# Kernel tuning notes

Measured on AMD Instinct MI355X. Metric: run time of the kernel, lower is better.

## Reference

```python
import jax, jax.numpy as jnp
import numpy as np

D_MODEL = 1024
NUM_HEADS = 16
D_HEAD = D_MODEL // NUM_HEADS


def rotate_half(x):
    half = x.shape[-1] // 2
    x1, x2 = x[..., :half], x[..., half:]
    return jnp.concatenate((-x2, x1), axis=-1)


def rope_cos_sin(seq_len, d_head, dtype):
    # inv_freq over even dims of d_head
    inv_freq = 1.0 / (10000.0 ** (jnp.arange(0, d_head, 2, dtype=jnp.float32) / d_head))
    t = jnp.arange(seq_len, dtype=jnp.float32)
    freqs = jnp.einsum('i,j->ij', t, inv_freq)        # [L, d_head/2]
    emb = jnp.concatenate((freqs, freqs), axis=-1)    # [L, d_head]
    return jnp.cos(emb).astype(dtype), jnp.sin(emb).astype(dtype)


def setup_inputs() -> dict:
    key = jax.random.key(0)
    ks = jax.random.split(key, 9)
    B, L = 2, 2048
    s = 1.0 / np.sqrt(D_MODEL)
    return {
        'x': jax.random.normal(ks[0], (B, L, D_MODEL), dtype=jnp.float32),
        'Wq': jax.random.normal(ks[1], (D_MODEL, D_MODEL), dtype=jnp.float32) * s,
        'bq': jax.random.normal(ks[2], (D_MODEL,), dtype=jnp.float32) * 0.02,
        'Wk': jax.random.normal(ks[3], (D_MODEL, D_MODEL), dtype=jnp.float32) * s,
        'bk': jax.random.normal(ks[4], (D_MODEL,), dtype=jnp.float32) * 0.02,
        'Wv': jax.random.normal(ks[5], (D_MODEL, D_MODEL), dtype=jnp.float32) * s,
        'bv': jax.random.normal(ks[6], (D_MODEL,), dtype=jnp.float32) * 0.02,
        'Wo': jax.random.normal(ks[7], (D_MODEL, D_MODEL), dtype=jnp.float32) * s,
        'bo': jax.random.normal(ks[8], (D_MODEL,), dtype=jnp.float32) * 0.02,
    }


def reference(x, Wq, bq, Wk, bk, Wv, bv, Wo, bo):
    B, L, D = x.shape
    H, Dh = NUM_HEADS, D_HEAD
    scale = Dh ** -0.5

    # projections: torch Linear is x @ W.T + b; here W stored as [in, out]-like
    # square matrices, so treat Wq etc. directly as x @ Wq + bq.
    q = (x @ Wq + bq).reshape(B, L, H, Dh).transpose(0, 2, 1, 3)  # [B,H,L,Dh]
    k = (x @ Wk + bk).reshape(B, L, H, Dh).transpose(0, 2, 1, 3)
    v = (x @ Wv + bv).reshape(B, L, H, Dh).transpose(0, 2, 1, 3)

    cos, sin = rope_cos_sin(L, Dh, x.dtype)  # [L, Dh]
    cos = cos[None, None]  # [1,1,L,Dh]
    sin = sin[None, None]
    q = q * cos + rotate_half(q) * sin
    k = k * cos + rotate_half(k) * sin

    attn = jnp.einsum('bhqd,bhkd->bhqk', q, k) * scale  # [B,H,L,L]
    attn = jax.nn.softmax(attn, axis=-1)
    out = jnp.einsum('bhqk,bhkd->bhqd', attn, v)        # [B,H,L,Dh]
    out = out.transpose(0, 2, 1, 3).reshape(B, L, D)
    return out @ Wo + bo
```

## Files before the change

kernel.cpp:

```cpp
#include <hip/hip_runtime.h>
#include <cmath>

#define D_MODEL  1024
#define NHEADS   16
#define DHEAD    64
#define BATCH    2
#define SEQ      2048
#define MROWS    (BATCH * SEQ)
#define HALF_DH  32
#define BHTOT    (BATCH * NHEADS)
#define QROWS    (BHTOT * SEQ)

typedef __attribute__((ext_vector_type(8))) short short8;
typedef __attribute__((ext_vector_type(4))) float f32x4;
typedef __attribute__((ext_vector_type(16))) float f32x16;

#define MFMA16(A,B,C) __builtin_amdgcn_mfma_f32_16x16x32_bf16(A,B,C,0,0,0)
#define MFMA32(A,B,C) __builtin_amdgcn_mfma_f32_32x32x16_bf16(A,B,C,0,0,0)

__device__ __forceinline__ unsigned short f2bf(float f) {
    unsigned int u = __float_as_uint(f);
    u += 0x7fffu + ((u >> 16) & 1u);
    return (unsigned short)(u >> 16);
}

__device__ __forceinline__ void gload_lds16(const void* g, void* l) {
    __builtin_amdgcn_global_load_lds(
        (const __attribute__((address_space(1))) unsigned int*)g,
        (__attribute__((address_space(3))) unsigned int*)l,
        16, 0, 0);
}

__global__ __launch_bounds__(256)
void prep_kernel(const float* __restrict__ x,
                 const float* __restrict__ Wq, const float* __restrict__ Wk,
                 const float* __restrict__ Wv, const float* __restrict__ Wo,
                 unsigned short* __restrict__ xb,
                 unsigned short* __restrict__ wqT, unsigned short* __restrict__ wkT,
                 unsigned short* __restrict__ wvT, unsigned short* __restrict__ woT,
                 float* __restrict__ cosT, float* __restrict__ sinT)
{
    __shared__ unsigned short T[64][68];
    const int bid = blockIdx.x;
    const int tid = threadIdx.x;

    if (bid < 4096) {
        int i = bid * 256 + tid;
        float4 v = ((const float4*)x)[i];
        ushort4 o;
        o.x = f2bf(v.x); o.y = f2bf(v.y); o.z = f2bf(v.z); o.w = f2bf(v.w);
        ((ushort4*)xb)[i] = o;
    } else if (bid < 5120) {
        int b2 = bid - 4096;
        int z  = b2 >> 8;
        int bx = (b2 & 255) >> 4;
        int by = b2 & 15;
        const float* W; unsigned short* Wt;
        switch (z) {
            case 0:  W = Wq; Wt = wqT; break;
            case 1:  W = Wk; Wt = wkT; break;
            case 2:  W = Wv; Wt = wvT; break;
            default: W = Wo; Wt = woT; break;
        }
        const int k0 = bx * 64, n0 = by * 64;
        const int r = tid >> 4, cq = tid & 15;
        #pragma unroll
        for (int p = 0; p < 4; ++p) {
            int kk = r + 16 * p;
            float4 vv = *(const float4*)&W[(size_t)(k0 + kk) * D_MODEL + n0 + cq * 4];
            T[cq * 4 + 0][kk] = f2bf(vv.x);
            T[cq * 4 + 1][kk] = f2bf(vv.y);
            T[cq * 4 + 2][kk] = f2bf(vv.z);
            T[cq * 4 + 3][kk] = f2bf(vv.w);
        }
        __syncthreads();
        #pragma unroll
        for (int p = 0; p < 4; ++p) {
            int n = r + 16 * p;
            ushort4 ov;
            ov.x = T[n][cq * 4 + 0]; ov.y = T[n][cq * 4 + 1];
            ov.z = T[n][cq * 4 + 2]; ov.w = T[n][cq * 4 + 3];
            *(ushort4*)&Wt[(size_t)(n0 + n) * D_MODEL + k0 + cq * 4] = ov;
        }
    } else {
        int idx = (bid - 5120) * 256 + tid;
        int l = idx >> 5;
        int j = idx & 31;
        float inv = powf(10000.0f, -(float)(2 * j) / (float)DHEAD);
        float ang = (float)l * inv;
        cosT[idx] = cosf(ang);
        sinT[idx] = sinf(ang);
    }
}

__global__ __launch_bounds__(256)
void qkv_proj_kernel(const unsigned short* __restrict__ A,
                     const unsigned short* __restrict__ wqT, const unsigned short* __restrict__ wkT,
                     const unsigned short* __restrict__ wvT,
                     const float* __restrict__ bq, const float* __restrict__ bk,
                     const float* __restrict__ bv,
                     const float* __restrict__ cosT, const float* __restrict__ sinT,
                     unsigned short* __restrict__ qb, unsigned short* __restrict__ kb,
                     unsigned short* __restrict__ vtb)
{
    __shared__ unsigned short SMEM[128 * 64 + 64 * 64];
    unsigned short* As = SMEM;
    unsigned short* Bs = SMEM + 128 * 64;

    const int z = blockIdx.z;
    const unsigned short* Bt = (z == 0) ? wqT : (z == 1) ? wkT : wvT;
    const float* bias = (z == 0) ? bq : (z == 1) ? bk : bv;

    const int tid = threadIdx.x;
    const int w = tid >> 6, ln = tid & 63;
    const int c = ln & 15, g = ln >> 4;
    const int bm = blockIdx.x * 128, bn = blockIdx.y * 64;
    const int srow = ln >> 3, sblk = ln & 7;

    f32x4 acc[2][4];
    #pragma unroll
    for (int mi = 0; mi < 2; ++mi)
        #pragma unroll
        for (int ni = 0; ni < 4; ++ni) acc[mi][ni] = (f32x4){0.f, 0.f, 0.f, 0.f};

    for (int k0 = 0; k0 < D_MODEL; k0 += 64) {
        __syncthreads();
        #pragma unroll
        for (int i = 0; i < 4; ++i) {
            int chunk = w * 4 + i;
            int row = chunk * 8 + srow;
            int gcol = (sblk ^ (row & 7)) * 8;
            gload_lds16(&A[(size_t)(bm + row) * D_MODEL + k0 + gcol], &As[chunk * 512]);
        }
        #pragma unroll
        for (int i = 0; i < 2; ++i) {
            int chunk = w * 2 + i;
            int row = chunk * 8 + srow;
            int gcol = (sblk ^ (row & 7)) * 8;
            gload_lds16(&Bt[(size_t)(bn + row) * D_MODEL + k0 + gcol], &Bs[chunk * 512]);
        }
        __syncthreads();

        #pragma unroll
        for (int ks = 0; ks < 2; ++ks) {
            const int koff = (ks * 32 + g * 8) ^ ((c & 7) * 8);
            short8 af[2];
            #pragma unroll
            for (int mi = 0; mi < 2; ++mi)
                af[mi] = *(const short8*)&As[(w * 32 + mi * 16 + c) * 64 + koff];
            #pragma unroll
            for (int ni = 0; ni < 4; ++ni) {
                short8 bfr = *(const short8*)&Bs[(ni * 16 + c) * 64 + koff];
                #pragma unroll
                for (int mi = 0; mi < 2; ++mi)
                    acc[mi][ni] = MFMA16(af[mi], bfr, acc[mi][ni]);
            }
        }
    }

    float bv4[4];
    #pragma unroll
    for (int ni = 0; ni < 4; ++ni) bv4[ni] = bias[bn + ni * 16 + c];

    if (z < 2) {
        unsigned short* op = z ? kb : qb;
        const int hy = blockIdx.y;
        #pragma unroll
        for (int mi = 0; mi < 2; ++mi) {
            #pragma unroll
            for (int r = 0; r < 4; ++r) {
                const int m = bm + w * 32 + mi * 16 + g * 4 + r;
                const int b = m >> 11, ll = m & (SEQ - 1);
                float v[4];
                #pragma unroll
                for (int ni = 0; ni < 4; ++ni) v[ni] = acc[mi][ni][r] + bv4[ni];
                #pragma unroll
                for (int ni = 0; ni < 2; ++ni) {
                    int d = ni * 16 + c;
                    float co = cosT[ll * HALF_DH + d];
                    float si = sinT[ll * HALF_DH + d];
                    float lo = v[ni], hi = v[ni + 2];
                    v[ni]     = lo * co - hi * si;
                    v[ni + 2] = hi * co + lo * si;
                }
                unsigned short* dst = op + ((size_t)(b * NHEADS + hy) * SEQ + ll) * DHEAD;
                #pragma unroll
                for (int ni = 0; ni < 4; ++ni) dst[ni * 16 + c] = f2bf(v[ni]);
            }
        }
    } else {
        unsigned short (*T)[136] = (unsigned short(*)[136])SMEM;
        __syncthreads();
        #pragma unroll
        for (int mi = 0; mi < 2; ++mi)
            #pragma unroll
            for (int r = 0; r < 4; ++r)
                #pragma unroll
                for (int ni = 0; ni < 4; ++ni)
                    T[ni * 16 + c][w * 32 + mi * 16 + g * 4 + r] = f2bf(acc[mi][ni][r] + bv4[ni]);
        __syncthreads();
        const int b  = bm >> 11;
        const int l0 = bm & (SEQ - 1);
        const int bh = b * NHEADS + blockIdx.y;
        unsigned short* Vo = vtb + (size_t)bh * DHEAD * SEQ;
        #pragma unroll
        for (int it = 0; it < 4; ++it) {
            int row  = (tid >> 4) + it * 16;
            int col8 = tid & 15;
            uint4 val = *(const uint4*)&T[row][col8 * 8];
            *(uint4*)&Vo[(size_t)row * SEQ + l0 + col8 * 8] = val;
        }
    }
}

__global__ __launch_bounds__(256)
void outproj_kernel(const unsigned short* __restrict__ A, const unsigned short* __restrict__ Bt,
                    const float* __restrict__ bias, float* __restrict__ out)
{
    __shared__ unsigned short As[128 * 64];
    __shared__ unsigned short Bs[64 * 64];
    const int tid = threadIdx.x;
    const int w = tid >> 6, ln = tid & 63;
    const int c = ln & 15, g = ln >> 4;
    const int bm = blockIdx.x * 128, bn = blockIdx.y * 64;
    const int srow = ln >> 3, sblk = ln & 7;

    f32x4 acc[2][4];
    #pragma unroll
    for (int mi = 0; mi < 2; ++mi)
        #pragma unroll
        for (int ni = 0; ni < 4; ++ni) acc[mi][ni] = (f32x4){0.f, 0.f, 0.f, 0.f};

    for (int k0 = 0; k0 < D_MODEL; k0 += 64) {
        __syncthreads();
        #pragma unroll
        for (int i = 0; i < 4; ++i) {
            int chunk = w * 4 + i;
            int row = chunk * 8 + srow;
            int gcol = (sblk ^ (row & 7)) * 8;
            gload_lds16(&A[(size_t)(bm + row) * D_MODEL + k0 + gcol], &As[chunk * 512]);
        }
        #pragma unroll
        for (int i = 0; i < 2; ++i) {
            int chunk = w * 2 + i;
            int row = chunk * 8 + srow;
            int gcol = (sblk ^ (row & 7)) * 8;
            gload_lds16(&Bt[(size_t)(bn + row) * D_MODEL + k0 + gcol], &Bs[chunk * 512]);
        }
        __syncthreads();

        #pragma unroll
        for (int ks = 0; ks < 2; ++ks) {
            const int koff = (ks * 32 + g * 8) ^ ((c & 7) * 8);
            short8 af[2];
            #pragma unroll
            for (int mi = 0; mi < 2; ++mi)
                af[mi] = *(const short8*)&As[(w * 32 + mi * 16 + c) * 64 + koff];
            #pragma unroll
            for (int ni = 0; ni < 4; ++ni) {
                short8 bfr = *(const short8*)&Bs[(ni * 16 + c) * 64 + koff];
                #pragma unroll
                for (int mi = 0; mi < 2; ++mi)
                    acc[mi][ni] = MFMA16(af[mi], bfr, acc[mi][ni]);
            }
        }
    }

    float bv4[4];
    #pragma unroll
    for (int ni = 0; ni < 4; ++ni) bv4[ni] = bias[bn + ni * 16 + c];
    #pragma unroll
    for (int mi = 0; mi < 2; ++mi)
        #pragma unroll
        for (int r = 0; r < 4; ++r) {
            const int m = bm + w * 32 + mi * 16 + g * 4 + r;
            #pragma unroll
            for (int ni = 0; ni < 4; ++ni)
                out[(size_t)m * D_MODEL + bn + ni * 16 + c] = acc[mi][ni][r] + bv4[ni];
        }
}

__global__ __launch_bounds__(256, 4)
void attn_mfma32_kernel(const unsigned short* __restrict__ Q, const unsigned short* __restrict__ K,
                        const unsigned short* __restrict__ Vt, unsigned short* __restrict__ O,
                        float* __restrict__ accP, float* __restrict__ ml, int nsplit)
{
    __shared__ unsigned short Ks[2][64 * 64];
    __shared__ unsigned short Vs[2][64 * 64];
    const int tid = threadIdx.x;
    const int w = tid >> 6, ln = tid & 63;
    const int ql = ln & 31;
    const int h  = ln >> 5;
    const int bh = blockIdx.y;
    const int q  = blockIdx.x * 128 + w * 32 + ql;
    const int split = blockIdx.z;
    const int ntile = SEQ / (64 * nsplit);
    const int kt0 = split * (SEQ / nsplit);
    const float SC = 0.125f * 1.44269504088896340736f;
    const int srow = ln >> 3, sblk = ln & 7;

    const unsigned short* Qb = Q  + (size_t)bh * SEQ * DHEAD;
    const unsigned short* Kb = K  + (size_t)bh * SEQ * DHEAD;
    const unsigned short* Vb = Vt + (size_t)bh * DHEAD * SEQ;

    short8 qf[4];
    #pragma unroll
    for (int dk = 0; dk < 4; ++dk)
        qf[dk] = *(const short8*)&Qb[(size_t)q * DHEAD + dk * 16 + h * 8];

    short8 onesF;
    #pragma unroll
    for (int i = 0; i < 8; ++i) onesF[i] = (short)0x3F80;

    int offk[4];
    #pragma unroll
    for (int t = 0; t < 4; ++t) offk[t] = ((2 * t + h) ^ (ql & 7)) * 8;
    const int rA = ql * 64, rB = (32 + ql) * 64;

    f32x16 accO0, accO1, accS;
    #pragma unroll
    for (int r = 0; r < 16; ++r) { accO0[r] = 0.f; accO1[r] = 0.f; accS[r] = 0.f; }
    float mst = -1e30f;

    #pragma unroll
    for (int i = 0; i < 2; ++i) {
        int chunk = w * 2 + i;
        int row = chunk * 8 + srow;
        int gcol = (sblk ^ (row & 7)) * 8;
        gload_lds16(&Kb[(size_t)(kt0 + row) * DHEAD + gcol], &Ks[0][chunk * 512]);
        gload_lds16(&Vb[(size_t)row * SEQ + kt0 + gcol],     &Vs[0][chunk * 512]);
    }
    __syncthreads();

    int cur = 0;
    for (int it = 0; it < ntile; ++it) {
        const int kt = kt0 + it * 64;
        if (it + 1 < ntile) {
            #pragma unroll
            for (int i = 0; i < 2; ++i) {
                int chunk = w * 2 + i;
                int row = chunk * 8 + srow;
                int gcol = (sblk ^ (row & 7)) * 8;
                gload_lds16(&Kb[(size_t)(kt + 64 + row) * DHEAD + gcol], &Ks[cur ^ 1][chunk * 512]);
                gload_lds16(&Vb[(size_t)row * SEQ + kt + 64 + gcol],     &Vs[cur ^ 1][chunk * 512]);
            }
        }

        f32x16 s0, s1;
        #pragma unroll
        for (int r = 0; r < 16; ++r) { s0[r] = 0.f; s1[r] = 0.f; }
        #pragma unroll
        for (int dk = 0; dk < 4; ++dk) {
            short8 kf0 = *(const short8*)&Ks[cur][rA + offk[dk]];
            short8 kf1 = *(const short8*)&Ks[cur][rB + offk[dk]];
            s0 = MFMA32(kf0, qf[dk], s0);
            s1 = MFMA32(kf1, qf[dk], s1);
        }

        float a0 = fmaxf(fmaxf(s0[0], s0[1]), s0[2]);
        float a1 = fmaxf(fmaxf(s0[3], s0[4]), s0[5]);
        float a2 = fmaxf(fmaxf(s0[6], s0[7]), s0[8]);
        float a3 = fmaxf(fmaxf(s0[9], s0[10]), s0[11]);
        float a4 = fmaxf(fmaxf(s0[12], s0[13]), s0[14]);
        float a5 = fmaxf(fmaxf(s0[15], s1[0]), s1[1]);
        float a6 = fmaxf(fmaxf(s1[2], s1[3]), s1[4]);
        float a7 = fmaxf(fmaxf(s1[5], s1[6]), s1[7]);
        float a8 = fmaxf(fmaxf(s1[8], s1[9]), s1[10]);
        float a9 = fmaxf(fmaxf(s1[11], s1[12]), s1[13]);
        float aA = fmaxf(s1[14], s1[15]);
        float b0 = fmaxf(fmaxf(a0, a1), a2);
        float b1 = fmaxf(fmaxf(a3, a4), a5);
        float b2 = fmaxf(fmaxf(a6, a7), a8);
        float b3 = fmaxf(a9, aA);
        float mx = fmaxf(fmaxf(fmaxf(b0, b1), b2), b3);
        mx = fmaxf(mx, __shfl_xor(mx, 32));

        const float mn = fmaxf(mst, mx);
        const float rsc = exp2f((mst - mn) * SC);
        #pragma unroll
        for (int r = 0; r < 16; ++r) { accO0[r] *= rsc; accO1[r] *= rsc; }
        accS[0] *= rsc;
        mst = mn;

        #pragma unroll
        for (int r = 0; r < 16; ++r) {
            s0[r] = exp2f((s0[r] - mst) * SC);
            s1[r] = exp2f((s1[r] - mst) * SC);
        }

        short8 pf[4];
        #define REPACK_T(T, SV)                                                          \
        {                                                                                \
            unsigned int wA0, wA1, wB0, wB1;                                             \
            asm("v_cvt_pk_bf16_f32 %0, %1, %2" : "=v"(wA0)                               \
                : "v"((SV)[8 * ((T) & 1) + 0]), "v"((SV)[8 * ((T) & 1) + 1]));           \
            asm("v_cvt_pk_bf16_f32 %0, %1, %2" : "=v"(wA1)                               \
                : "v"((SV)[8 * ((T) & 1) + 2]), "v"((SV)[8 * ((T) & 1) + 3]));           \
            asm("v_cvt_pk_bf16_f32 %0, %1, %2" : "=v"(wB0)                               \
                : "v"((SV)[8 * ((T) & 1) + 4]), "v"((SV)[8 * ((T) & 1) + 5]));           \
            asm("v_cvt_pk_bf16_f32 %0, %1, %2" : "=v"(wB1)                               \
                : "v"((SV)[8 * ((T) & 1) + 6]), "v"((SV)[8 * ((T) & 1) + 7]));           \
            asm("v_permlane32_swap_b32 %0, %1" : "+v"(wA0), "+v"(wB0));                  \
            asm("v_permlane32_swap_b32 %0, %1" : "+v"(wA1), "+v"(wB1));                  \
            union { short8 v; unsigned int u[4]; } tmp;                                  \
            tmp.u[0] = wA0; tmp.u[1] = wA1; tmp.u[2] = wB0; tmp.u[3] = wB1;              \
            pf[T] = tmp.v;                                                               \
        }
        REPACK_T(0, s0) REPACK_T(1, s0) REPACK_T(2, s1) REPACK_T(3, s1)
        #undef REPACK_T

        #pragma unroll
        for (int t = 0; t < 4; ++t) {
            short8 vf0 = *(const short8*)&Vs[cur][rA + offk[t]];
            short8 vf1 = *(const short8*)&Vs[cur][rB + offk[t]];
            accS  = MFMA32(onesF, pf[t], accS);
            accO0 = MFMA32(vf0, pf[t], accO0);
            accO1 = MFMA32(vf1, pf[t], accO1);
        }

        __syncthreads();
        cur ^= 1;
    }

    const float accL = accS[0];
    if (nsplit == 1) {
        const int b = bh >> 4, hh = bh & 15;
        const float inv = 1.0f / accL;
        unsigned short* dst = O + ((size_t)(b * SEQ + q)) * D_MODEL + hh * DHEAD;
        #define EPI(ACC, DC)                                                             \
        {                                                                                \
            _Pragma("unroll")                                                            \
            for (int rq = 0; rq < 4; ++rq) {                                             \
                float a0 = (ACC)[4 * rq + 0] * inv, a1 = (ACC)[4 * rq + 1] * inv;        \
                float a2 = (ACC)[4 * rq + 2] * inv, a3 = (ACC)[4 * rq + 3] * inv;        \
                unsigned int p0, p1;                                                     \
                asm("v_cvt_pk_bf16_f32 %0, %1, %2" : "=v"(p0) : "v"(a0), "v"(a1));       \
                asm("v_cvt_pk_bf16_f32 %0, %1, %2" : "=v"(p1) : "v"(a2), "v"(a3));       \
                uint2 pk; pk.x = p0; pk.y = p1;                                          \
                *(uint2*)(dst + 32 * (DC) + 8 * rq + 4 * h) = pk;                        \
            }                                                                            \
        }
        EPI(accO0, 0) EPI(accO1, 1)
        #undef EPI
    } else {
        float* base = accP + ((size_t)(split * BHTOT + bh) * SEQ + q) * 64;
        #pragma unroll
        for (int rq = 0; rq < 4; ++rq) {
            float4 v0, v1;
            v0.x = accO0[4 * rq + 0]; v0.y = accO0[4 * rq + 1];
            v0.z = accO0[4 * rq + 2]; v0.w = accO0[4 * rq + 3];
            v1.x = accO1[4 * rq + 0]; v1.y = accO1[4 * rq + 1];
            v1.z = accO1[4 * rq + 2]; v1.w = accO1[4 * rq + 3];
            *(float4*)&base[8 * rq + 4 * h]      = v0;
            *(float4*)&base[32 + 8 * rq + 4 * h] = v1;
        }
        if (h == 0) {
            float2 v; v.x = mst; v.y = accL;
            ((float2*)ml)[(size_t)(split * BHTOT + bh) * SEQ + q] = v;
        }
    }
}

__global__ __launch_bounds__(256)
void combine2_kernel(const float* __restrict__ accP, const float* __restrict__ ml,
                     unsigned short* __restrict__ ob)
{
    const float SC = 0.125f * 1.44269504088896340736f;
    int t = blockIdx.x * 256 + threadIdx.x;
    int d4  = (t & 15) * 4;
    int bhq = t >> 4;
    const float2* ML = (const float2*)ml;
    float2 m0 = ML[bhq];
    float2 m1 = ML[(size_t)QROWS + bhq];
    float M  = fmaxf(m0.x, m1.x);
    float w0 = exp2f((m0.x - M) * SC);
    float w1 = exp2f((m1.x - M) * SC);
    float inv = 1.0f / (w0 * m0.y + w1 * m1.y);
    float4 a0 = *(const float4*)&accP[(size_t)bhq * 64 + d4];
    float4 a1 = *(const float4*)&accP[(size_t)QROWS * 64 + (size_t)bhq * 64 + d4];
    float o0 = (a0.x * w0 + a1.x * w1) * inv;
    float o1 = (a0.y * w0 + a1.y * w1) * inv;
    float o2 = (a0.z * w0 + a1.z * w1) * inv;
    float o3 = (a0.w * w0 + a1.w * w1) * inv;
    int bh = bhq >> 11, q = bhq & (SEQ - 1);
    int b = bh >> 4, hh = bh & 15;
    ushort4 ov;
    ov.x = f2bf(o0); ov.y = f2bf(o1); ov.z = f2bf(o2); ov.w = f2bf(o3);
    *(ushort4*)&ob[((size_t)(b * SEQ + q)) * D_MODEL + hh * DHEAD + d4] = ov;
}

extern "C" void kernel_launch(void* const* d_in, const int* in_sizes, int n_in,
                              void* d_out, int out_size, void* d_ws, size_t ws_size,
                              hipStream_t stream)
{
    const float* x  = (const float*)d_in[0];
    const float* Wq = (const float*)d_in[1];
    const float* bq = (const float*)d_in[2];
    const float* Wk = (const float*)d_in[3];
    const float* bk = (const float*)d_in[4];
    const float* Wv = (const float*)d_in[5];
    const float* bv = (const float*)d_in[6];
    const float* Wo = (const float*)d_in[7];
    const float* bo = (const float*)d_in[8];

    char* p = (char*)d_ws;
    float* cosT = (float*)p;            p += (size_t)SEQ * HALF_DH * 4;
    float* sinT = (float*)p;            p += (size_t)SEQ * HALF_DH * 4;
    unsigned short* xb  = (unsigned short*)p; p += (size_t)MROWS * D_MODEL * 2;
    unsigned short* wqT = (unsigned short*)p; p += (size_t)D_MODEL * D_MODEL * 2;
    unsigned short* wkT = (unsigned short*)p; p += (size_t)D_MODEL * D_MODEL * 2;
    unsigned short* wvT = (unsigned short*)p; p += (size_t)D_MODEL * D_MODEL * 2;
    unsigned short* woT = (unsigned short*)p; p += (size_t)D_MODEL * D_MODEL * 2;
    unsigned short* qb  = (unsigned short*)p; p += (size_t)MROWS * D_MODEL * 2;
    unsigned short* kb  = (unsigned short*)p; p += (size_t)MROWS * D_MODEL * 2;
    unsigned short* vtb = (unsigned short*)p; p += (size_t)MROWS * D_MODEL * 2;
    unsigned short* ob  = (unsigned short*)p; p += (size_t)MROWS * D_MODEL * 2;
    float* accP = (float*)p;            p += (size_t)2 * QROWS * 64 * 4;
    float* ml   = (float*)p;            p += (size_t)2 * QROWS * 2 * 4;
    size_t need2 = (size_t)(p - (char*)d_ws);
    const int nsplit = (ws_size >= need2) ? 2 : 1;

    prep_kernel<<<5376, 256, 0, stream>>>(x, Wq, Wk, Wv, Wo,
                                          xb, wqT, wkT, wvT, woT, cosT, sinT);

    qkv_proj_kernel<<<dim3(MROWS / 128, D_MODEL / 64, 3), 256, 0, stream>>>(
        xb, wqT, wkT, wvT, bq, bk, bv, cosT, sinT, qb, kb, vtb);

    attn_mfma32_kernel<<<dim3(SEQ / 128, BHTOT, nsplit), 256, 0, stream>>>(
        qb, kb, vtb, ob, accP, ml, nsplit);

    if (nsplit == 2)
        combine2_kernel<<<(QROWS * 16) / 256, 256, 0, stream>>>(accP, ml, ob);

    outproj_kernel<<<dim3(MROWS / 128, D_MODEL / 64), 256, 0, stream>>>(ob, woT, bo, (float*)d_out);
}
```

Measured before the change: 151.9 us.

## Widen projection GEMM tiles to 128 columns and skip rescale when max grows little

The QKV and output projection kernels now compute 128x128 tiles instead of 128x64, doubling accumulators per wave and halving the grid, so each A tile loaded into LDS feeds twice as much MFMA work. The epilogues are restructured to handle two heads per block, including the V transpose via shared memory done per head. Separately, the attention kernel now skips the online-softmax rescale unless some lane's max grows by more than a threshold, which avoids many multiplies but lets exponent arguments exceed zero by up to that bound. The larger tile raises register and LDS use and halves the block count, which can reduce occupancy.

```diff
diff --git a/kernel.cpp b/kernel.cpp
--- a/kernel.cpp
+++ b/kernel.cpp
@@ -103,7 +103,7 @@
                      unsigned short* __restrict__ qb, unsigned short* __restrict__ kb,
                      unsigned short* __restrict__ vtb)
 {
-    __shared__ unsigned short SMEM[128 * 64 + 64 * 64];
+    __shared__ unsigned short SMEM[128 * 64 + 128 * 64];
     unsigned short* As = SMEM;
     unsigned short* Bs = SMEM + 128 * 64;
 
@@ -114,14 +114,14 @@
     const int tid = threadIdx.x;
     const int w = tid >> 6, ln = tid & 63;
     const int c = ln & 15, g = ln >> 4;
-    const int bm = blockIdx.x * 128, bn = blockIdx.y * 64;
+    const int bm = blockIdx.x * 128, bn = blockIdx.y * 128;
     const int srow = ln >> 3, sblk = ln & 7;
 
-    f32x4 acc[2][4];
+    f32x4 acc[2][8];
     #pragma unroll
     for (int mi = 0; mi < 2; ++mi)
         #pragma unroll
-        for (int ni = 0; ni < 4; ++ni) acc[mi][ni] = (f32x4){0.f, 0.f, 0.f, 0.f};
+        for (int ni = 0; ni < 8; ++ni) acc[mi][ni] = (f32x4){0.f, 0.f, 0.f, 0.f};
 
     for (int k0 = 0; k0 < D_MODEL; k0 += 64) {
         __syncthreads();
@@ -133,8 +133,8 @@
             gload_lds16(&A[(size_t)(bm + row) * D_MODEL + k0 + gcol], &As[chunk * 512]);
         }
         #pragma unroll
-        for (int i = 0; i < 2; ++i) {
-            int chunk = w * 2 + i;
+        for (int i = 0; i < 4; ++i) {
+            int chunk = w * 4 + i;
             int row = chunk * 8 + srow;
             int gcol = (sblk ^ (row & 7)) * 8;
             gload_lds16(&Bt[(size_t)(bn + row) * D_MODEL + k0 + gcol], &Bs[chunk * 512]);
@@ -149,7 +149,7 @@
             for (int mi = 0; mi < 2; ++mi)
                 af[mi] = *(const short8*)&As[(w * 32 + mi * 16 + c) * 64 + koff];
             #pragma unroll
-            for (int ni = 0; ni < 4; ++ni) {
+            for (int ni = 0; ni < 8; ++ni) {
                 short8 bfr = *(const short8*)&Bs[(ni * 16 + c) * 64 + koff];
                 #pragma unroll
                 for (int mi = 0; mi < 2; ++mi)
@@ -158,57 +158,69 @@
         }
     }
 
-    float bv4[4];
-    #pragma unroll
-    for (int ni = 0; ni < 4; ++ni) bv4[ni] = bias[bn + ni * 16 + c];
+    float bv8[8];
+    #pragma unroll
+    for (int ni = 0; ni < 8; ++ni) bv8[ni] = bias[bn + ni * 16 + c];
 
     if (z < 2) {
         unsigned short* op = z ? kb : qb;
-        const int hy = blockIdx.y;
+        const int h0 = bn >> 6;
         #pragma unroll
         for (int mi = 0; mi < 2; ++mi) {
             #pragma unroll
             for (int r = 0; r < 4; ++r) {
                 const int m = bm + w * 32 + mi * 16 + g * 4 + r;
                 const int b = m >> 11, ll = m & (SEQ - 1);
-                float v[4];
+                float v[8];
                 #pragma unroll
-                for (int ni = 0; ni < 4; ++ni) v[ni] = acc[mi][ni][r] + bv4[ni];
+                for (int ni = 0; ni < 8; ++ni) v[ni] = acc[mi][ni][r] + bv8[ni];
                 #pragma unroll
-                for (int ni = 0; ni < 2; ++ni) {
-                    int d = ni * 16 + c;
-                    float co = cosT[ll * HALF_DH + d];
-                    float si = sinT[ll * HALF_DH + d];
-                    float lo = v[ni], hi = v[ni + 2];
-                    v[ni]     = lo * co - hi * si;
-                    v[ni + 2] = hi * co + lo * si;
+                for (int hp = 0; hp < 2; ++hp) {
+                    #pragma unroll
+                    for (int nj = 0; nj < 2; ++nj) {
+                        int d = nj * 16 + c;
+                        float co = cosT[ll * HALF_DH + d];
+                        float si = sinT[ll * HALF_DH + d];
+                        float lo = v[hp * 4 + nj], hi = v[hp * 4 + nj + 2];
+                        v[hp * 4 + nj]     = lo * co - hi * si;
+                        v[hp * 4 + nj + 2] = hi * co + lo * si;
+                    }
                 }
-                unsigned short* dst = op + ((size_t)(b * NHEADS + hy) * SEQ + ll) * DHEAD;
                 #pragma unroll
-                for (int ni = 0; ni < 4; ++ni) dst[ni * 16 + c] = f2bf(v[ni]);
+                for (int hp = 0; hp < 2; ++hp) {
+                    unsigned short* dst = op
+                        + ((size_t)(b * NHEADS + h0 + hp) * SEQ + ll) * DHEAD;
+                    #pragma unroll
+                    for (int nj = 0; nj < 4; ++nj) dst[nj * 16 + c] = f2bf(v[hp * 4 + nj]);
+                }
             }
         }
     } else {
         unsigned short (*T)[136] = (unsigned short(*)[136])SMEM;
-        __syncthreads();
-        #pragma unroll
-        for (int mi = 0; mi < 2; ++mi)
-            #pragma unroll
-            for (int r = 0; r < 4; ++r)
-                #pragma unroll
-                for (int ni = 0; ni < 4; ++ni)
-                    T[ni * 16 + c][w * 32 + mi * 16 + g * 4 + r] = f2bf(acc[mi][ni][r] + bv4[ni]);
-        __syncthreads();
         const int b  = bm >> 11;
         const int l0 = bm & (SEQ - 1);
-        const int bh = b * NHEADS + blockIdx.y;
-        unsigned short* Vo = vtb + (size_t)bh * DHEAD * SEQ;
-        #pragma unroll
-        for (int it = 0; it < 4; ++it) {
-            int row  = (tid >> 4) + it * 16;
-            int col8 = tid & 15;
-            uint4 val = *(const uint4*)&T[row][col8 * 8];
-            *(uint4*)&Vo[(size_t)row * SEQ + l0 + col8 * 8] = val;
+        const int h0 = bn >> 6;
+        #pragma unroll
+        for (int hp = 0; hp < 2; ++hp) {
+            __syncthreads();
+            #pragma unroll
+            for (int mi = 0; mi < 2; ++mi)
+                #pragma unroll
+                for (int r = 0; r < 4; ++r)
+                    #pragma unroll
+                    for (int nj = 0; nj < 4; ++nj)
+                        T[nj * 16 + c][w * 32 + mi * 16 + g * 4 + r]
+                            = f2bf(acc[mi][hp * 4 + nj][r] + bv8[hp * 4 + nj]);
+            __syncthreads();
+            const int bh = b * NHEADS + h0 + hp;
+            unsigned short* Vo = vtb + (size_t)bh * DHEAD * SEQ;
+            #pragma unroll
+            for (int it = 0; it < 4; ++it) {
+                int row  = (tid >> 4) + it * 16;
+                int col8 = tid & 15;
+                uint4 val = *(const uint4*)&T[row][col8 * 8];
+                *(uint4*)&Vo[(size_t)row * SEQ + l0 + col8 * 8] = val;
+            }
         }
     }
 }
@@ -218,18 +230,18 @@
                     const float* __restrict__ bias, float* __restrict__ out)
 {
     __shared__ unsigned short As[128 * 64];
-    __shared__ unsigned short Bs[64 * 64];
+    __shared__ unsigned short Bs[128 * 64];
     const int tid = threadIdx.x;
     const int w = tid >> 6, ln = tid & 63;
     const int c = ln & 15, g = ln >> 4;
-    const int bm = blockIdx.x * 128, bn = blockIdx.y * 64;
+    const int bm = blockIdx.x * 128, bn = blockIdx.y * 128;
     const int srow = ln >> 3, sblk = ln & 7;
 
-    f32x4 acc[2][4];
+    f32x4 acc[2][8];
     #pragma unroll
     for (int mi = 0; mi < 2; ++mi)
         #pragma unroll
-        for (int ni = 0; ni < 4; ++ni) acc[mi][ni] = (f32x4){0.f, 0.f, 0.f, 0.f};
+        for (int ni = 0; ni < 8; ++ni) acc[mi][ni] = (f32x4){0.f, 0.f, 0.f, 0.f};
 
     for (int k0 = 0; k0 < D_MODEL; k0 += 64) {
         __syncthreads();
@@ -241,8 +253,8 @@
             gload_lds16(&A[(size_t)(bm + row) * D_MODEL + k0 + gcol], &As[chunk * 512]);
         }
         #pragma unroll
-        for (int i = 0; i < 2; ++i) {
-            int chunk = w * 2 + i;
+        for (int i = 0; i < 4; ++i) {
+            int chunk = w * 4 + i;
             int row = chunk * 8 + srow;
             int gcol = (sblk ^ (row & 7)) * 8;
             gload_lds16(&Bt[(size_t)(bn + row) * D_MODEL + k0 + gcol], &Bs[chunk * 512]);
@@ -257,7 +269,7 @@
             for (int mi = 0; mi < 2; ++mi)
                 af[mi] = *(const short8*)&As[(w * 32 + mi * 16 + c) * 64 + koff];
             #pragma unroll
-            for (int ni = 0; ni < 4; ++ni) {
+            for (int ni = 0; ni < 8; ++ni) {
                 short8 bfr = *(const short8*)&Bs[(ni * 16 + c) * 64 + koff];
                 #pragma unroll
                 for (int mi = 0; mi < 2; ++mi)
@@ -266,17 +278,17 @@
         }
     }
 
-    float bv4[4];
-    #pragma unroll
-    for (int ni = 0; ni < 4; ++ni) bv4[ni] = bias[bn + ni * 16 + c];
+    float bv8[8];
+    #pragma unroll
+    for (int ni = 0; ni < 8; ++ni) bv8[ni] = bias[bn + ni * 16 + c];
     #pragma unroll
     for (int mi = 0; mi < 2; ++mi)
         #pragma unroll
         for (int r = 0; r < 4; ++r) {
             const int m = bm + w * 32 + mi * 16 + g * 4 + r;
             #pragma unroll
-            for (int ni = 0; ni < 4; ++ni)
-                out[(size_t)m * D_MODEL + bn + ni * 16 + c] = acc[mi][ni][r] + bv4[ni];
+            for (int ni = 0; ni < 8; ++ni)
+                out[(size_t)m * D_MODEL + bn + ni * 16 + c] = acc[mi][ni][r] + bv8[ni];
         }
 }
 
@@ -375,12 +387,15 @@
         float mx = fmaxf(fmaxf(fmaxf(b0, b1), b2), b3);
         mx = fmaxf(mx, __shfl_xor(mx, 32));
 
-        const float mn = fmaxf(mst, mx);
-        const float rsc = exp2f((mst - mn) * SC);
-        #pragma unroll
-        for (int r = 0; r < 16; ++r) { accO0[r] *= rsc; accO1[r] *= rsc; }
-        accS[0] *= rsc;
-        mst = mn;
+        const float grow = (mx - mst) * SC;
+        if (!__all(grow <= 4.0f)) {
+            const float mn = fmaxf(mst, mx);
+            const float rsc = exp2f((mst - mn) * SC);
+            #pragma unroll
+            for (int r = 0; r < 16; ++r) { accO0[r] *= rsc; accO1[r] *= rsc; }
+            accS[0] *= rsc;
+            mst = mn;
+        }
 
         #pragma unroll
         for (int r = 0; r < 16; ++r) {
@@ -523,7 +538,7 @@
     prep_kernel<<<5376, 256, 0, stream>>>(x, Wq, Wk, Wv, Wo,
                                           xb, wqT, wkT, wvT, woT, cosT, sinT);
 
-    qkv_proj_kernel<<<dim3(MROWS / 128, D_MODEL / 64, 3), 256, 0, stream>>>(
+    qkv_proj_kernel<<<dim3(MROWS / 128, D_MODEL / 128, 3), 256, 0, stream>>>(
         xb, wqT, wkT, wvT, bq, bk, bv, cosT, sinT, qb, kb, vtb);
 
     attn_mfma32_kernel<<<dim3(SEQ / 128, BHTOT, nsplit), 256, 0, stream>>>(
@@ -532,5 +547,5 @@
     if (nsplit == 2)
         combine2_kernel<<<(QROWS * 16) / 256, 256, 0, stream>>>(accP, ml, ob);
 
-    outproj_kernel<<<dim3(MROWS / 128, D_MODEL / 64), 256, 0, stream>>>(ob, woT, bo, (float*)d_out);
-}
+    outproj_kernel<<<dim3(MROWS / 128, D_MODEL / 128), 256, 0, stream>>>(ob, woT, bo, (float*)d_out);
+}
```

Result: no change. 154.2 us (+1.5%).
